# Performance work log

Hardware: AMD Instinct MI355X
Metric: run time of the kernel (lower is better)

## Reference

```python
import jax, jax.numpy as jnp
import numpy as np

N = 10000
E = 160000


def _lin(key, fi, fo):
    kw, kb = jax.random.split(key)
    W = jax.random.normal(kw, (fi, fo), dtype=jnp.float32) * 0.02
    b = jnp.zeros((fo,), dtype=jnp.float32)
    return W, b


def setup_inputs() -> dict:
    key = jax.random.key(0)
    ks = jax.random.split(key, 20)
    inp = {}
    inp['x'] = jax.random.normal(ks[0], (N, 2048), dtype=jnp.float32)
    src = jax.random.randint(ks[1], (E,), 0, N)
    dst = jax.random.randint(ks[2], (E,), 0, N)
    inp['edge_index'] = jnp.stack([src, dst]).astype(jnp.int64)
    dims = [(2048, 1024), (1024, 2048), (2048, 1024), (1024, 2048)]
    ki = 3
    for li, (fi, fo) in enumerate(dims, start=1):
        for name in ('q', 'k', 'v', 's'):
            W, b = _lin(ks[ki], fi, fo)
            ki += 1
            inp[f'W{li}{name}'] = W
            inp[f'b{li}{name}'] = b
    return inp


def _tconv(x, src, dst, Wq, bq, Wk, bk, Wv, bv, Ws, bs):
    # PyG TransformerConv, heads=1: per-edge attention j->i, softmax over
    # incoming edges of each target node i, plus root (skip) linear.
    q = x @ Wq + bq                      # [N, C]
    k = x @ Wk + bk
    v = x @ Wv + bv
    C = q.shape[-1]
    logits = jnp.sum(q[dst] * k[src], axis=-1) / jnp.sqrt(jnp.float32(C))  # [E]
    m = jax.ops.segment_max(logits, dst, num_segments=N)   # per-node max
    m = jnp.where(jnp.isfinite(m), m, 0.0)                  # isolated nodes
    e = jnp.exp(logits - m[dst])
    s = jax.ops.segment_sum(e, dst, num_segments=N)
    alpha = e / (s[dst] + 1e-16)                            # [E]
    agg = jax.ops.segment_sum(v[src] * alpha[:, None], dst, num_segments=N)
    return agg + x @ Ws + bs


def reference(x, edge_index,
              W1q, b1q, W1k, b1k, W1v, b1v, W1s, b1s,
              W2q, b2q, W2k, b2k, W2v, b2v, W2s, b2s,
              W3q, b3q, W3k, b3k, W3v, b3v, W3s, b3s,
              W4q, b4q, W4k, b4k, W4v, b4v, W4s, b4s):
    src, dst = edge_index[0], edge_index[1]
    h1 = jax.nn.elu(_tconv(x, src, dst, W1q, b1q, W1k, b1k, W1v, b1v, W1s, b1s))
    h2 = _tconv(h1, src, dst, W2q, b2q, W2k, b2k, W2v, b2v, W2s, b2s)
    h3 = jax.nn.elu(_tconv(h2, src, dst, W3q, b3q, W3k, b3k, W3v, b3v, W3s, b3s))
    out = _tconv(h3, src, dst, W4q, b4q, W4k, b4k, W4v, b4v, W4s, b4s)
    return out
```

## Files before the change

kernel.cpp:

```cpp
#include <hip/hip_runtime.h>
#include <cmath>
#include <cstddef>
#include <cstdint>

typedef __attribute__((ext_vector_type(8))) _Float16 half8_t;
typedef __attribute__((ext_vector_type(4))) _Float16 half4_t;
typedef __attribute__((ext_vector_type(2))) _Float16 half2_t;
typedef __attribute__((ext_vector_type(4))) float f32x4;

__device__ __forceinline__ float dot2f16(half2_t a, half2_t b, float c) {
#if __has_builtin(__builtin_amdgcn_fdot2)
  return __builtin_amdgcn_fdot2(a, b, c, false);
#else
  return c + (float)a.x * (float)b.x + (float)a.y * (float)b.y;
#endif
}

__device__ __forceinline__ void gload16(const unsigned short* g,
                                        unsigned short* l) {
  __builtin_amdgcn_global_load_lds(
      (const __attribute__((address_space(1))) unsigned int*)g,
      (__attribute__((address_space(3))) unsigned int*)l, 16, 0, 0);
}

__global__ __launch_bounds__(256) void cast_f16_k(
    const float* __restrict__ in, unsigned short* __restrict__ out, size_t n4) {
  size_t i = (size_t)blockIdx.x * blockDim.x + threadIdx.x;
  if (i >= n4) return;
  float4 v = ((const float4*)in)[i];
  half4_t h;
  h.x = (_Float16)v.x;
  h.y = (_Float16)v.y;
  h.z = (_Float16)v.z;
  h.w = (_Float16)v.w;
  ((half4_t*)out)[i] = h;
}

__global__ __launch_bounds__(256) void transp_f16_k(
    const float* __restrict__ W0, const float* __restrict__ W1,
    const float* __restrict__ W2, const float* __restrict__ W3,
    unsigned short* __restrict__ T, int K, int C) {
  __shared__ float t[32][33];
  const int m = blockIdx.z;
  const float* W = (m == 0) ? W0 : (m == 1) ? W1 : (m == 2) ? W2 : W3;
  _Float16* th = (_Float16*)T + (size_t)m * C * K;
  int k0 = blockIdx.x * 32, c0 = blockIdx.y * 32;
  int tx = threadIdx.x & 31, ty = threadIdx.x >> 5;
#pragma unroll
  for (int r = 0; r < 4; ++r)
    t[ty + r * 8][tx] = W[(size_t)(k0 + ty + r * 8) * C + c0 + tx];
  __syncthreads();
#pragma unroll
  for (int r = 0; r < 4; ++r) {
    int c = ty + r * 8;
    th[(size_t)(c0 + c) * K + k0 + tx] = (_Float16)t[tx][c];
  }
}

__global__ __launch_bounds__(512) void gemm_f16_k(
    const unsigned short* __restrict__ Ab, const unsigned short* __restrict__ Wt,
    const float* __restrict__ bq, const float* __restrict__ bk,
    const float* __restrict__ bv, const float* __restrict__ bs,
    unsigned short* __restrict__ Qh, unsigned short* __restrict__ Kh,
    unsigned short* __restrict__ Vh, float* __restrict__ S, int M, int K,
    int C, int NX, int NY) {
  __shared__ unsigned short lds[3][12288];

  const int nwg = NX * NY;
  const int bid = blockIdx.x;
  const int qq = nwg >> 3, rr = nwg & 7;
  const int xcd = bid & 7, idx = bid >> 3;
  const int wgid =
      (xcd < rr ? xcd * (qq + 1) : rr * (qq + 1) + (xcd - rr) * qq) + idx;
  const int by = wgid % NY, bx = wgid / NY;

  const int bm = bx * 256, n0 = by * 128;
  const int kind = n0 / C;
  const int tid = threadIdx.x;
  const int lane = tid & 63, w = tid >> 6;
  const int wm = w >> 1, wn = w & 1;
  const int fr = lane & 15, kg = lane >> 4;

  const int srow = w * 16 + (lane >> 2);
  const int soff = (lane & 3) * 8;
  const size_t ga0 = (size_t)min(bm + srow, M - 1) * K + soff;
  const size_t ga1 = (size_t)min(bm + srow + 128, M - 1) * K + soff;
  const size_t gb0 = (size_t)(n0 + srow) * K + soff;
  const int la0 = w * 512;
  const int la1 = 4096 + w * 512;
  const int lb0 = 8192 + w * 512;

  f32x4 acc[4][4];
#pragma unroll
  for (int i = 0; i < 4; ++i)
#pragma unroll
    for (int j = 0; j < 4; ++j) acc[i][j] = (f32x4)0.f;

  auto STAGE = [&](int buf, int ko) {
    gload16(Ab + ga0 + ko, &lds[buf][la0]);
    gload16(Ab + ga1 + ko, &lds[buf][la1]);
    gload16(Wt + gb0 + ko, &lds[buf][lb0]);
  };

  const int T = K / 32;
  STAGE(0, 0);
  STAGE(1, 32);

  int buf = 0;
  for (int t = 0; t < T; ++t) {
    if (t + 1 < T)
      asm volatile("s_waitcnt vmcnt(3)" ::: "memory");
    else
      asm volatile("s_waitcnt vmcnt(0)" ::: "memory");
    __builtin_amdgcn_s_barrier();
    asm volatile("" ::: "memory");
    if (t + 2 < T) {
      int nb = buf + 2;
      if (nb >= 3) nb -= 3;
      STAGE(nb, (t + 2) * 32);
    }
    const unsigned short* As = lds[buf];
    const unsigned short* Bs = lds[buf] + 8192;
    half8_t ah[4], bh[4];
#pragma unroll
    for (int i = 0; i < 4; ++i) {
      ah[i] = *(const half8_t*)(As + (wm * 64 + i * 16 + fr) * 32 + kg * 8);
      bh[i] = *(const half8_t*)(Bs + (wn * 64 + i * 16 + fr) * 32 + kg * 8);
    }
#pragma unroll
    for (int i = 0; i < 4; ++i)
#pragma unroll
      for (int j = 0; j < 4; ++j)
        acc[i][j] = __builtin_amdgcn_mfma_f32_16x16x32_f16(ah[i], bh[j],
                                                           acc[i][j], 0, 0, 0);
    asm volatile("s_waitcnt lgkmcnt(0)" ::: "memory");
    buf = (buf == 2) ? 0 : buf + 1;
  }

  const float* bptr = (kind == 0) ? bq : (kind == 1) ? bk : (kind == 2) ? bv : bs;
  const int cbase = (n0 - kind * C) + wn * 64;
  float bvv[4];
#pragma unroll
  for (int j = 0; j < 4; ++j) bvv[j] = bptr[cbase + j * 16 + fr];

  unsigned short* obu = (kind == 0) ? Qh : (kind == 1) ? Kh : Vh;
  _Float16* ob = (_Float16*)obu;
#pragma unroll
  for (int i = 0; i < 4; ++i) {
#pragma unroll
    for (int r = 0; r < 4; ++r) {
      int gr = bm + wm * 64 + i * 16 + kg * 4 + r;
      if (gr < M) {
        if (kind == 3) {
#pragma unroll
          for (int j = 0; j < 4; ++j)
            S[(size_t)gr * C + cbase + j * 16 + fr] = acc[i][j][r] + bvv[j];
        } else {
#pragma unroll
          for (int j = 0; j < 4; ++j)
            ob[(size_t)gr * C + cbase + j * 16 + fr] =
                (_Float16)(acc[i][j][r] + bvv[j]);
        }
      }
    }
  }
}

__global__ __launch_bounds__(256) void attn_fused2_k(
    const unsigned short* __restrict__ Qh, const unsigned short* __restrict__ Kh,
    const unsigned short* __restrict__ Vh, const int* __restrict__ rowptr,
    const int* __restrict__ csr_src, float* __restrict__ gscratch,
    float* __restrict__ skipio, unsigned short* __restrict__ Hb, int C,
    float scale, int do_elu, int writeH) {
  __shared__ _Float16 qs[2048];
  __shared__ float ebuf[512];
  __shared__ int ssrc[512];
  __shared__ float wred[8];
  const int i = blockIdx.x;
  const int tid = threadIdx.x;
  const int lane = tid & 63, wid = tid >> 6;
  const int beg = rowptr[i], end = rowptr[i + 1];
  const int deg = end - beg;
  const bool sm = (deg <= 512);

  for (int c0 = tid * 4; c0 < C; c0 += 1024)
    *(uint2*)&qs[c0] = *(const uint2*)(Qh + (size_t)i * C + c0);
  if (sm)
    for (int p = tid; p < deg; p += 256) ssrc[p] = csr_src[beg + p];
  if (tid < 8) wred[tid] = (tid < 4) ? -INFINITY : 0.f;
  __syncthreads();

  if (deg > 0) {
    float wmaxv = -INFINITY;
    for (int ep = wid; ep < deg; ep += 4) {
      int s = sm ? ssrc[ep] : csr_src[beg + ep];
      const unsigned short* kr = Kh + (size_t)s * C;
      float sum = 0.f;
      for (int c0 = lane * 8; c0 < C; c0 += 512) {
        uint4 kk = *(const uint4*)(kr + c0);
        uint4 qq4 = *(const uint4*)&qs[c0];
        const half2_t* kp = (const half2_t*)&kk;
        const half2_t* qp = (const half2_t*)&qq4;
        sum = dot2f16(kp[0], qp[0], sum);
        sum = dot2f16(kp[1], qp[1], sum);
        sum = dot2f16(kp[2], qp[2], sum);
        sum = dot2f16(kp[3], qp[3], sum);
      }
#pragma unroll
      for (int o = 32; o; o >>= 1) sum += __shfl_xor(sum, o);
      float lg = sum * scale;
      if (lane == 0) {
        if (sm) ebuf[ep] = lg; else gscratch[beg + ep] = lg;
      }
      wmaxv = fmaxf(wmaxv, lg);
    }
    if (lane == 0) wred[wid] = wmaxv;
    __syncthreads();
    float m = fmaxf(fmaxf(wred[0], wred[1]), fmaxf(wred[2], wred[3]));

    float part = 0.f;
    for (int ep = tid; ep < deg; ep += 256) {
      float lg = sm ? ebuf[ep] : gscratch[beg + ep];
      float e = expf(lg - m);
      if (sm) ebuf[ep] = e; else gscratch[beg + ep] = e;
      part += e;
    }
#pragma unroll
    for (int o = 32; o; o >>= 1) part += __shfl_xor(part, o);
    if (lane == 0) wred[4 + wid] = part;
  }
  __syncthreads();

  float total = wred[4] + wred[5] + wred[6] + wred[7];
  float denom = 1.f / (total + 1e-16f);
  const int cpt = C >> 8;
  const int col0 = tid * cpt;
  float acc[8];
#pragma unroll
  for (int j = 0; j < 8; ++j) acc[j] = 0.f;

  for (int ep = 0; ep < deg; ++ep) {
    float a = (sm ? ebuf[ep] : gscratch[beg + ep]) * denom;
    int s = sm ? ssrc[ep] : csr_src[beg + ep];
    const unsigned short* vr = Vh + (size_t)s * C + col0;
    if (cpt == 4) {
      ushort4 pv = *(const ushort4*)vr;
      const _Float16* ph = (const _Float16*)&pv;
#pragma unroll
      for (int u = 0; u < 4; ++u) acc[u] = fmaf(a, (float)ph[u], acc[u]);
    } else {
      uint4 pv = *(const uint4*)vr;
      const _Float16* ph = (const _Float16*)&pv;
#pragma unroll
      for (int u = 0; u < 8; ++u) acc[u] = fmaf(a, (float)ph[u], acc[u]);
    }
  }

  float* srow = skipio + (size_t)i * C + col0;
#pragma unroll
  for (int v4 = 0; v4 < 2; ++v4) {
    if (v4 * 4 < cpt) {
      float4 o = *(const float4*)(srow + v4 * 4);
      o.x += acc[v4 * 4 + 0];
      o.y += acc[v4 * 4 + 1];
      o.z += acc[v4 * 4 + 2];
      o.w += acc[v4 * 4 + 3];
      if (do_elu) {
        o.x = o.x > 0.f ? o.x : expm1f(o.x);
        o.y = o.y > 0.f ? o.y : expm1f(o.y);
        o.z = o.z > 0.f ? o.z : expm1f(o.z);
        o.w = o.w > 0.f ? o.w : expm1f(o.w);
      }
      if (writeH) {
        half4_t h;
        h.x = (_Float16)o.x;
        h.y = (_Float16)o.y;
        h.z = (_Float16)o.z;
        h.w = (_Float16)o.w;
        *(half4_t*)((_Float16*)Hb + (size_t)i * C + col0 + v4 * 4) = h;
      } else {
        *(float4*)(srow + v4 * 4) = o;
      }
    }
  }
}

__global__ void count_deg_k(const int* __restrict__ dst, int E,
                            int* __restrict__ cnt) {
  int e = blockIdx.x * blockDim.x + threadIdx.x;
  if (e < E) atomicAdd(&cnt[dst[e]], 1);
}

__global__ void scan_k(const int* __restrict__ cnt, int* __restrict__ rowptr,
                       int N) {
  __shared__ int part[1024];
  int t = threadIdx.x;
  int per = (N + 1023) >> 10;
  int base = t * per;
  int s = 0;
  for (int i = 0; i < per; ++i) {
    int idx = base + i;
    if (idx < N) s += cnt[idx];
  }
  part[t] = s;
  __syncthreads();
  for (int off = 1; off < 1024; off <<= 1) {
    int v = (t >= off) ? part[t - off] : 0;
    __syncthreads();
    part[t] += v;
    __syncthreads();
  }
  int run = part[t] - s;
  for (int i = 0; i < per; ++i) {
    int idx = base + i;
    if (idx < N) {
      rowptr[idx] = run;
      run += cnt[idx];
    }
  }
  if (t == 1023) rowptr[N] = part[1023];
}

__global__ void scatter_csr_k(const int* __restrict__ src,
                              const int* __restrict__ dst, int E,
                              const int* __restrict__ rowptr,
                              int* __restrict__ fill,
                              int* __restrict__ csr_src) {
  int e = blockIdx.x * blockDim.x + threadIdx.x;
  if (e >= E) return;
  int d = dst[e];
  int pos = rowptr[d] + atomicAdd(&fill[d], 1);
  csr_src[pos] = src[e];
}

extern "C" void kernel_launch(void* const* d_in, const int* in_sizes, int n_in,
                              void* d_out, int out_size, void* d_ws,
                              size_t ws_size, hipStream_t stream) {
  const float* x = (const float*)d_in[0];
  const int* eidx = (const int*)d_in[1];
  const int N = in_sizes[0] / 2048;
  const int E = in_sizes[1] / 2;
  const int* srcA = eidx;
  const int* dstA = eidx + E;
  float* dout = (float*)d_out;

  char* p = (char*)d_ws;
  auto alloc = [&](size_t bytes) {
    void* r = (void*)p;
    p += (bytes + 255) & ~(size_t)255;
    return r;
  };

  float* logits = (float*)alloc((size_t)E * 4);
  int* rowptr = (int*)alloc((size_t)(N + 1) * 4);
  int* cnt = (int*)alloc((size_t)N * 4);
  int* fill = (int*)alloc((size_t)N * 4);
  int* csr_src = (int*)alloc((size_t)E * 4);

  hipMemsetAsync(cnt, 0, (size_t)N * 4, stream);
  hipMemsetAsync(fill, 0, (size_t)N * 4, stream);
  count_deg_k<<<(E + 255) / 256, 256, 0, stream>>>(dstA, E, cnt);
  scan_k<<<1, 1024, 0, stream>>>(cnt, rowptr, N);
  scatter_csr_k<<<(E + 255) / 256, 256, 0, stream>>>(srcA, dstA, E, rowptr,
                                                     fill, csr_src);

  const size_t szH = (size_t)N * 2048 * 2;
  const size_t szWt = (size_t)4 * 1024 * 2048 * 2;

  unsigned short* Hb = (unsigned short*)alloc(szH);
  unsigned short* Qh = (unsigned short*)alloc(szH);
  unsigned short* Kh = (unsigned short*)alloc(szH);
  unsigned short* Vh = (unsigned short*)alloc(szH);
  unsigned short* Wt = (unsigned short*)alloc(szWt);

  const int fi[4] = {2048, 1024, 2048, 1024};
  const int fo[4] = {1024, 2048, 1024, 2048};
  const int elu[4] = {1, 0, 1, 0};

  cast_f16_k<<<(int)(((size_t)N * 2048 / 4 + 255) / 256), 256, 0, stream>>>(
      x, Hb, (size_t)N * 2048 / 4);

  for (int L = 0; L < 4; ++L) {
    const int K = fi[L], C = fo[L];
    const int b = 2 + L * 8;
    const float scale = (float)(1.0 / sqrt((double)C));
    transp_f16_k<<<dim3(K / 32, C / 32, 4), 256, 0, stream>>>(
        (const float*)d_in[b + 0], (const float*)d_in[b + 2],
        (const float*)d_in[b + 4], (const float*)d_in[b + 6], Wt, K, C);
    const int NX = (N + 255) / 256;
    const int NY = 4 * C / 128;
    gemm_f16_k<<<NX * NY, 512, 0, stream>>>(
        Hb, Wt, (const float*)d_in[b + 1], (const float*)d_in[b + 3],
        (const float*)d_in[b + 5], (const float*)d_in[b + 7], Qh, Kh, Vh, dout,
        N, K, C, NX, NY);
    attn_fused2_k<<<N, 256, 0, stream>>>(Qh, Kh, Vh, rowptr, csr_src, logits,
                                         dout, Hb, C, scale, elu[L],
                                         L < 3 ? 1 : 0);
  }
}
```

Before: 1.515 ms.

## Swizzle GEMM LDS layout, unroll attention edge loops, hoist weight transposes

The GEMM now XOR-swizzles the 16-byte column chunk within each 32-element LDS row, on both the global-to-LDS staging and the fragment reads, to reduce LDS bank conflicts. In the attention kernel's fast path, each wave computes two edge logits per iteration and the value aggregation processes four edges at a time, giving more loads in flight. The four weight-transpose kernels are moved ahead of the layer loop into separate buffers, which removes the dependency between each layer's transpose and its GEMM at the cost of extra memory. The swizzle has to match exactly between the staging and the read side or the GEMM results will be wrong.

```diff
diff --git a/kernel.cpp b/kernel.cpp
--- a/kernel.cpp
+++ b/kernel.cpp
@@ -82,7 +82,7 @@
   const int fr = lane & 15, kg = lane >> 4;
 
   const int srow = w * 16 + (lane >> 2);
-  const int soff = (lane & 3) * 8;
+  const int soff = (((lane & 3) ^ ((lane >> 2) & 3))) * 8;
   const size_t ga0 = (size_t)min(bm + srow, M - 1) * K + soff;
   const size_t ga1 = (size_t)min(bm + srow + 128, M - 1) * K + soff;
   const size_t gb0 = (size_t)(n0 + srow) * K + soff;
@@ -106,6 +106,7 @@
   STAGE(0, 0);
   STAGE(1, 32);
 
+  const int rka = (kg ^ (fr & 3)) * 8;
   int buf = 0;
   for (int t = 0; t < T; ++t) {
     if (t + 1 < T)
@@ -124,8 +125,8 @@
     half8_t ah[4], bh[4];
 #pragma unroll
     for (int i = 0; i < 4; ++i) {
-      ah[i] = *(const half8_t*)(As + (wm * 64 + i * 16 + fr) * 32 + kg * 8);
-      bh[i] = *(const half8_t*)(Bs + (wn * 64 + i * 16 + fr) * 32 + kg * 8);
+      ah[i] = *(const half8_t*)(As + (wm * 64 + i * 16 + fr) * 32 + rka);
+      bh[i] = *(const half8_t*)(Bs + (wn * 64 + i * 16 + fr) * 32 + rka);
     }
 #pragma unroll
     for (int i = 0; i < 4; ++i)
@@ -192,27 +193,60 @@
 
   if (deg > 0) {
     float wmaxv = -INFINITY;
-    for (int ep = wid; ep < deg; ep += 4) {
-      int s = sm ? ssrc[ep] : csr_src[beg + ep];
-      const unsigned short* kr = Kh + (size_t)s * C;
-      float sum = 0.f;
-      for (int c0 = lane * 8; c0 < C; c0 += 512) {
-        uint4 kk = *(const uint4*)(kr + c0);
-        uint4 qq4 = *(const uint4*)&qs[c0];
-        const half2_t* kp = (const half2_t*)&kk;
-        const half2_t* qp = (const half2_t*)&qq4;
-        sum = dot2f16(kp[0], qp[0], sum);
-        sum = dot2f16(kp[1], qp[1], sum);
-        sum = dot2f16(kp[2], qp[2], sum);
-        sum = dot2f16(kp[3], qp[3], sum);
-      }
-#pragma unroll
-      for (int o = 32; o; o >>= 1) sum += __shfl_xor(sum, o);
-      float lg = sum * scale;
-      if (lane == 0) {
-        if (sm) ebuf[ep] = lg; else gscratch[beg + ep] = lg;
-      }
-      wmaxv = fmaxf(wmaxv, lg);
+    if (sm) {
+      for (int ep = wid; ep < deg; ep += 8) {
+        const int e1 = ep + 4;
+        const bool h1 = e1 < deg;
+        int s0 = ssrc[ep];
+        int s1 = h1 ? ssrc[e1] : s0;
+        const unsigned short* kr0 = Kh + (size_t)s0 * C;
+        const unsigned short* kr1 = Kh + (size_t)s1 * C;
+        float su0 = 0.f, su1 = 0.f;
+        for (int c0 = lane * 8; c0 < C; c0 += 512) {
+          uint4 k0 = *(const uint4*)(kr0 + c0);
+          uint4 k1 = *(const uint4*)(kr1 + c0);
+          uint4 qv = *(const uint4*)&qs[c0];
+          const half2_t* kp0 = (const half2_t*)&k0;
+          const half2_t* kp1 = (const half2_t*)&k1;
+          const half2_t* qp = (const half2_t*)&qv;
+#pragma unroll
+          for (int u = 0; u < 4; ++u) {
+            su0 = dot2f16(kp0[u], qp[u], su0);
+            su1 = dot2f16(kp1[u], qp[u], su1);
+          }
+        }
+#pragma unroll
+        for (int o = 32; o; o >>= 1) {
+          su0 += __shfl_xor(su0, o);
+          su1 += __shfl_xor(su1, o);
+        }
+        float lg0 = su0 * scale;
+        float lg1 = h1 ? su1 * scale : -INFINITY;
+        if (lane == 0) {
+          ebuf[ep] = lg0;
+          if (h1) ebuf[e1] = lg1;
+        }
+        wmaxv = fmaxf(wmaxv, fmaxf(lg0, lg1));
+      }
+    } else {
+      for (int ep = wid; ep < deg; ep += 4) {
+        int s = csr_src[beg + ep];
+        const unsigned short* kr = Kh + (size_t)s * C;
+        float sum = 0.f;
+        for (int c0 = lane * 8; c0 < C; c0 += 512) {
+          uint4 kk = *(const uint4*)(kr + c0);
+          uint4 qv = *(const uint4*)&qs[c0];
+          const half2_t* kp = (const half2_t*)&kk;
+          const half2_t* qp = (const half2_t*)&qv;
+#pragma unroll
+          for (int u = 0; u < 4; ++u) sum = dot2f16(kp[u], qp[u], sum);
+        }
+#pragma unroll
+        for (int o = 32; o; o >>= 1) sum += __shfl_xor(sum, o);
+        float lg = sum * scale;
+        if (lane == 0) gscratch[beg + ep] = lg;
+        wmaxv = fmaxf(wmaxv, lg);
+      }
     }
     if (lane == 0) wred[wid] = wmaxv;
     __syncthreads();
@@ -239,20 +273,81 @@
 #pragma unroll
   for (int j = 0; j < 8; ++j) acc[j] = 0.f;
 
-  for (int ep = 0; ep < deg; ++ep) {
-    float a = (sm ? ebuf[ep] : gscratch[beg + ep]) * denom;
-    int s = sm ? ssrc[ep] : csr_src[beg + ep];
-    const unsigned short* vr = Vh + (size_t)s * C + col0;
-    if (cpt == 4) {
-      ushort4 pv = *(const ushort4*)vr;
-      const _Float16* ph = (const _Float16*)&pv;
-#pragma unroll
-      for (int u = 0; u < 4; ++u) acc[u] = fmaf(a, (float)ph[u], acc[u]);
+  if (sm) {
+    int ep = 0;
+    if (cpt == 8) {
+      for (; ep + 4 <= deg; ep += 4) {
+        float a0 = ebuf[ep] * denom, a1 = ebuf[ep + 1] * denom;
+        float a2 = ebuf[ep + 2] * denom, a3 = ebuf[ep + 3] * denom;
+        const unsigned short* v0 = Vh + (size_t)ssrc[ep] * C + col0;
+        const unsigned short* v1 = Vh + (size_t)ssrc[ep + 1] * C + col0;
+        const unsigned short* v2 = Vh + (size_t)ssrc[ep + 2] * C + col0;
+        const unsigned short* v3 = Vh + (size_t)ssrc[ep + 3] * C + col0;
+        uint4 p0 = *(const uint4*)v0, p1 = *(const uint4*)v1;
+        uint4 p2 = *(const uint4*)v2, p3 = *(const uint4*)v3;
+        const _Float16* h0 = (const _Float16*)&p0;
+        const _Float16* h1 = (const _Float16*)&p1;
+        const _Float16* h2 = (const _Float16*)&p2;
+        const _Float16* h3 = (const _Float16*)&p3;
+#pragma unroll
+        for (int u = 0; u < 8; ++u) {
+          acc[u] = fmaf(a0, (float)h0[u], acc[u]);
+          acc[u] = fmaf(a1, (float)h1[u], acc[u]);
+          acc[u] = fmaf(a2, (float)h2[u], acc[u]);
+          acc[u] = fmaf(a3, (float)h3[u], acc[u]);
+        }
+      }
+      for (; ep < deg; ++ep) {
+        float a = ebuf[ep] * denom;
+        uint4 pv = *(const uint4*)(Vh + (size_t)ssrc[ep] * C + col0);
+        const _Float16* ph = (const _Float16*)&pv;
+#pragma unroll
+        for (int u = 0; u < 8; ++u) acc[u] = fmaf(a, (float)ph[u], acc[u]);
+      }
     } else {
-      uint4 pv = *(const uint4*)vr;
-      const _Float16* ph = (const _Float16*)&pv;
-#pragma unroll
-      for (int u = 0; u < 8; ++u) acc[u] = fmaf(a, (float)ph[u], acc[u]);
+      for (; ep + 4 <= deg; ep += 4) {
+        float a0 = ebuf[ep] * denom, a1 = ebuf[ep + 1] * denom;
+        float a2 = ebuf[ep + 2] * denom, a3 = ebuf[ep + 3] * denom;
+        ushort4 p0 = *(const ushort4*)(Vh + (size_t)ssrc[ep] * C + col0);
+        ushort4 p1 = *(const ushort4*)(Vh + (size_t)ssrc[ep + 1] * C + col0);
+        ushort4 p2 = *(const ushort4*)(Vh + (size_t)ssrc[ep + 2] * C + col0);
+        ushort4 p3 = *(const ushort4*)(Vh + (size_t)ssrc[ep + 3] * C + col0);
+        const _Float16* h0 = (const _Float16*)&p0;
+        const _Float16* h1 = (const _Float16*)&p1;
+        const _Float16* h2 = (const _Float16*)&p2;
+        const _Float16* h3 = (const _Float16*)&p3;
+#pragma unroll
+        for (int u = 0; u < 4; ++u) {
+          acc[u] = fmaf(a0, (float)h0[u], acc[u]);
+          acc[u] = fmaf(a1, (float)h1[u], acc[u]);
+          acc[u] = fmaf(a2, (float)h2[u], acc[u]);
+          acc[u] = fmaf(a3, (float)h3[u], acc[u]);
+        }
+      }
+      for (; ep < deg; ++ep) {
+        float a = ebuf[ep] * denom;
+        ushort4 pv = *(const ushort4*)(Vh + (size_t)ssrc[ep] * C + col0);
+        const _Float16* ph = (const _Float16*)&pv;
+#pragma unroll
+        for (int u = 0; u < 4; ++u) acc[u] = fmaf(a, (float)ph[u], acc[u]);
+      }
+    }
+  } else {
+    for (int ep = 0; ep < deg; ++ep) {
+      float a = gscratch[beg + ep] * denom;
+      int s = csr_src[beg + ep];
+      const unsigned short* vr = Vh + (size_t)s * C + col0;
+      if (cpt == 4) {
+        ushort4 pv = *(const ushort4*)vr;
+        const _Float16* ph = (const _Float16*)&pv;
+#pragma unroll
+        for (int u = 0; u < 4; ++u) acc[u] = fmaf(a, (float)ph[u], acc[u]);
+      } else {
+        uint4 pv = *(const uint4*)vr;
+        const _Float16* ph = (const _Float16*)&pv;
+#pragma unroll
+        for (int u = 0; u < 8; ++u) acc[u] = fmaf(a, (float)ph[u], acc[u]);
+      }
     }
   }
 
@@ -371,7 +466,8 @@
   unsigned short* Qh = (unsigned short*)alloc(szH);
   unsigned short* Kh = (unsigned short*)alloc(szH);
   unsigned short* Vh = (unsigned short*)alloc(szH);
-  unsigned short* Wt = (unsigned short*)alloc(szWt);
+  unsigned short* Wt[4];
+  for (int L = 0; L < 4; ++L) Wt[L] = (unsigned short*)alloc(szWt);
 
   const int fi[4] = {2048, 1024, 2048, 1024};
   const int fo[4] = {1024, 2048, 1024, 2048};
@@ -379,18 +475,23 @@
 
   cast_f16_k<<<(int)(((size_t)N * 2048 / 4 + 255) / 256), 256, 0, stream>>>(
       x, Hb, (size_t)N * 2048 / 4);
+
+  for (int L = 0; L < 4; ++L) {
+    const int K = fi[L], C = fo[L];
+    const int b = 2 + L * 8;
+    transp_f16_k<<<dim3(K / 32, C / 32, 4), 256, 0, stream>>>(
+        (const float*)d_in[b + 0], (const float*)d_in[b + 2],
+        (const float*)d_in[b + 4], (const float*)d_in[b + 6], Wt[L], K, C);
+  }
 
   for (int L = 0; L < 4; ++L) {
     const int K = fi[L], C = fo[L];
     const int b = 2 + L * 8;
     const float scale = (float)(1.0 / sqrt((double)C));
-    transp_f16_k<<<dim3(K / 32, C / 32, 4), 256, 0, stream>>>(
-        (const float*)d_in[b + 0], (const float*)d_in[b + 2],
-        (const float*)d_in[b + 4], (const float*)d_in[b + 6], Wt, K, C);
     const int NX = (N + 255) / 256;
     const int NY = 4 * C / 128;
     gemm_f16_k<<<NX * NY, 512, 0, stream>>>(
-        Hb, Wt, (const float*)d_in[b + 1], (const float*)d_in[b + 3],
+        Hb, Wt[L], (const float*)d_in[b + 1], (const float*)d_in[b + 3],
         (const float*)d_in[b + 5], (const float*)d_in[b + 7], Qh, Kh, Vh, dout,
         N, K, C, NX, NY);
     attn_fused2_k<<<N, 256, 0, stream>>>(Qh, Kh, Vh, rowptr, csr_src, logits,
```

Result: faster. 1.461 ms (-3.5%).
